# Optimization experiments

Measured on AMD Instinct MI355X. Metric: run time of the kernel, lower is better.

Reference implementation:

```python
import jax, jax.numpy as jnp
import numpy as np

K = 20                      # kNN size (init kwarg k)
_BN_S = 1.0 / np.sqrt(1.0 + 1e-5)  # BatchNorm eval with running var=1, mean=0


def _edge_conv(f, W1, b1, g, be, W2, b2):
    # f: [B,N,C]. DynamicEdgeConv: kNN in feature space (self included, as in
    # torch_cluster.knn), message = MLP([x_i, x_j - x_i]), max aggregation.
    sq = jnp.sum(f * f, -1)
    d = sq[:, :, None] + sq[:, None, :] - 2.0 * jnp.einsum('bnc,bmc->bnm', f, f)
    _, idx = jax.lax.top_k(-d, K)                      # [B,N,K]
    fj = jax.vmap(lambda fb, ib: fb[ib])(f, idx)       # [B,N,K,C] neighbor gather
    fi = jnp.broadcast_to(f[:, :, None, :], fj.shape)
    msg = jnp.concatenate([fi, fj - fi], -1)           # [B,N,K,2C]
    h = jax.nn.relu((msg @ W1 + b1) * (g * _BN_S) + be)  # Linear -> BN(eval) -> ReLU
    h = h @ W2 + b2                                    # plain last MLP layer
    return jnp.max(h, axis=2)                          # max over K neighbors


def _forward(x, pos,
             c1_W1, c1_b1, c1_g, c1_be, c1_W2, c1_b2,
             c2_W1, c2_b1, c2_g, c2_be, c2_W2, c2_b2,
             c3_W1, c3_b1, c3_g, c3_be, c3_W2, c3_b2,
             m_W1, m_b1, m_W2, m_b2, m_W3, m_b3, m_W4, m_b4):
    x0 = jnp.concatenate([x, pos], -1)                 # [B,N,6]
    x1 = _edge_conv(x0, c1_W1, c1_b1, c1_g, c1_be, c1_W2, c1_b2)
    x2 = _edge_conv(x1, c2_W1, c2_b1, c2_g, c2_be, c2_W2, c2_b2)
    x3 = _edge_conv(x2, c3_W1, c3_b1, c3_g, c3_be, c3_W2, c3_b2)
    h = jnp.concatenate([x1, x2, x3], -1)              # [B,N,192]
    # head MLP: norm=None, dropout inactive at inference, plain last layer
    h = jax.nn.relu(h @ m_W1 + m_b1)
    h = jax.nn.relu(h @ m_W2 + m_b2)
    h = jax.nn.relu(h @ m_W3 + m_b3)
    out = h @ m_W4 + m_b4                              # [B,N,40]
    return jax.nn.log_softmax(out, -1)


def setup_inputs() -> dict:
    key = jax.random.key(0)
    ks = iter(jax.random.split(key, 40))

    def lin(cin, cout):
        W = jax.random.normal(next(ks), (cin, cout), jnp.float32) / np.sqrt(cin)
        b = jnp.zeros((cout,), jnp.float32)
        return W, b

    inp = {}
    inp['x'] = jax.random.normal(next(ks), (8, 4096, 3), jnp.float32)
    inp['pos'] = jax.random.normal(next(ks), (8, 4096, 3), jnp.float32)
    for i, cin in zip((1, 2, 3), (12, 128, 128)):      # 2*in_channels of each conv
        W1, b1 = lin(cin, 64)
        W2, b2 = lin(64, 64)
        inp[f'c{i}_W1'], inp[f'c{i}_b1'] = W1, b1
        inp[f'c{i}_g'] = jnp.ones((64,), jnp.float32)
        inp[f'c{i}_be'] = jnp.zeros((64,), jnp.float32)
        inp[f'c{i}_W2'], inp[f'c{i}_b2'] = W2, b2
    dims = [192, 1024, 256, 128, 40]
    for j in range(4):
        W, b = lin(dims[j], dims[j + 1])
        inp[f'm_W{j + 1}'], inp[f'm_b{j + 1}'] = W, b
    return inp


def reference(x, pos,
              c1_W1, c1_b1, c1_g, c1_be, c1_W2, c1_b2,
              c2_W1, c2_b1, c2_g, c2_be, c2_W2, c2_b2,
              c3_W1, c3_b1, c3_g, c3_be, c3_W2, c3_b2,
              m_W1, m_b1, m_W2, m_b2, m_W3, m_b3, m_W4, m_b4):
    return _forward(x, pos,
                    c1_W1, c1_b1, c1_g, c1_be, c1_W2, c1_b2,
                    c2_W1, c2_b1, c2_g, c2_be, c2_W2, c2_b2,
                    c3_W1, c3_b1, c3_g, c3_be, c3_W2, c3_b2,
                    m_W1, m_b1, m_W2, m_b2, m_W3, m_b3, m_W4, m_b4)
```

## Files before the change

### kernel.cpp

```cpp
#include <hip/hip_runtime.h>
#include <math.h>

#define KNN 20
#define NPTS 4096
#define NB 8

__device__ __forceinline__ bool lexless(float d1, int i1, float d2, int i2) {
    return d1 < d2 || (d1 == d2 && i1 < i2);
}

__global__ __launch_bounds__(256) void concat_kernel(const float* __restrict__ x,
                                                     const float* __restrict__ pos,
                                                     float* __restrict__ f0, int total) {
    int p = blockIdx.x * 256 + threadIdx.x;
    if (p < total) {
        f0[(size_t)p*6 + 0] = x[(size_t)p*3 + 0];
        f0[(size_t)p*6 + 1] = x[(size_t)p*3 + 1];
        f0[(size_t)p*6 + 2] = x[(size_t)p*3 + 2];
        f0[(size_t)p*6 + 3] = pos[(size_t)p*3 + 0];
        f0[(size_t)p*6 + 4] = pos[(size_t)p*3 + 1];
        f0[(size_t)p*6 + 5] = pos[(size_t)p*3 + 2];
    }
}

template<int C>
__global__ __launch_bounds__(256) void norm_kernel(const float* __restrict__ f, int ldf,
                                                   float* __restrict__ norms, int total) {
    int p = blockIdx.x * 256 + threadIdx.x;
    if (p >= total) return;
    const float* fp = f + (size_t)p * ldf;
    float s = 0.f;
    if constexpr ((C & 3) == 0) {
#pragma unroll
        for (int k = 0; k < C; k += 4) {
            float4 v = *(const float4*)(fp + k);
            s = fmaf(v.x, v.x, s); s = fmaf(v.y, v.y, s);
            s = fmaf(v.z, v.z, s); s = fmaf(v.w, v.w, s);
        }
    } else {
#pragma unroll
        for (int k = 0; k < C; ++k) s = fmaf(fp[k], fp[k], s);
    }
    norms[p] = s;
}

#define KCHAIN(ck_) do {                                                 \
    unsigned long long kc = (ck_);                                       \
    _Pragma("unroll")                                                    \
    for (int t = 0; t < KNN; ++t) {                                      \
        bool sw = kc < bk[t];                                            \
        unsigned long long nn = sw ? kc : bk[t];                         \
        unsigned long long oo = sw ? bk[t] : kc;                         \
        bk[t] = nn; kc = oo;                                             \
    }                                                                    \
} while (0)

#define PACKK(dv_, jv_, out_) do {                                       \
    unsigned pu = __float_as_uint(dv_);                                  \
    pu = (pu == 0x80000000u) ? 0u : pu;                    \
    pu ^= (unsigned)((int)pu >> 31) | 0x80000000u;                       \
    (out_) = ((unsigned long long)pu << 32) | (unsigned)(jv_);           \
} while (0)

#define PUSHF(dv_, jg_) do {                                             \
    if ((dv_) <= thr) {                                                  \
        pd5 = pd4; pj5 = pj4; pd4 = pd3; pj4 = pj3;                      \
        pd3 = pd2; pj3 = pj2; pd2 = pd1; pj2 = pj1;                      \
        pd1 = pd0; pj1 = pj0; pd0 = (dv_); pj0 = (jg_); ++cnt;           \
    }                                                                    \
} while (0)

#define FLUSHF() do {                                                    \
    if (cnt > 0) { unsigned long long k0_; PACKK(pd0, pj0, k0_); KCHAIN(k0_); } \
    if (cnt > 1) { unsigned long long k1_; PACKK(pd1, pj1, k1_); KCHAIN(k1_); } \
    if (cnt > 2) { unsigned long long k2_; PACKK(pd2, pj2, k2_); KCHAIN(k2_); } \
    if (cnt > 3) { unsigned long long k3_; PACKK(pd3, pj3, k3_); KCHAIN(k3_); } \
    if (cnt > 4) { unsigned long long k4_; PACKK(pd4, pj4, k4_); KCHAIN(k4_); } \
    if (cnt > 5) { unsigned long long k5_; PACKK(pd5, pj5, k5_); KCHAIN(k5_); } \
    cnt = 0;                                                             \
    unsigned hu_ = (unsigned)(bk[KNN - 1] >> 32);                        \
    atomicMin(&thrQ[q], hu_);                                            \
    hu_ = (hu_ & 0x80000000u) ? (hu_ ^ 0x80000000u) : ~hu_;              \
    thr = __uint_as_float(hu_);                                          \
} while (0)

#define KMERGE(ptr_) do {                                                \
    const unsigned long long* mp = (ptr_);                               \
    _Pragma("unroll 1")                                                  \
    for (int tm = 0; tm < KNN; ++tm) {                                   \
        unsigned long long mk = mp[tm];                                  \
        if (mk >= bk[KNN - 1]) break;                                    \
        KCHAIN(mk);                                                      \
    }                                                                    \
} while (0)

#define KSENTINEL 0xFF800000FFFFFFFFULL

template<int C>
__global__ __launch_bounds__(128, 2) void knn_tile_kernel(const float* __restrict__ f, int ldf,
                                                          const float* __restrict__ norms,
                                                          int* __restrict__ idx) {
    const int qb    = blockIdx.x * 32;
    const int b     = qb >> 12;
    const int qloc0 = qb & (NPTS - 1);
    const int tid   = threadIdx.x;
    const int q     = tid & 31;
    const int sub   = tid >> 5;
    const int tx    = tid & 15;
    const int ty    = tid >> 4;

    union __align__(16) SM {
        struct {
            float Qs[C][32];
            float Cs[C][64];
            float Ds[32][68];
        } a;
        unsigned long long md[32][2 * KNN + 1];
    };
    __shared__ SM sm;
    __shared__ unsigned thrQ[32];

    const float* fb = f + (size_t)b * NPTS * ldf;
    const float* nb = norms + (size_t)b * NPTS;

    if (tid < 32) thrQ[tid] = 0xFFFFFFFFu;

    if constexpr ((C & 15) == 0) {
        int m = tid >> 2, ko = (tid & 3) * 4;
        const float* src = fb + (size_t)(qloc0 + m) * ldf;
#pragma unroll
        for (int k4 = ko; k4 < C; k4 += 16) {
            float4 v = *(const float4*)(src + k4);
            sm.a.Qs[k4 + 0][m] = v.x; sm.a.Qs[k4 + 1][m] = v.y;
            sm.a.Qs[k4 + 2][m] = v.z; sm.a.Qs[k4 + 3][m] = v.w;
        }
    } else {
        for (int e = tid; e < C * 32; e += 128) {
            int k = e >> 5, m = e & 31;
            sm.a.Qs[k][m] = fb[(size_t)(qloc0 + m) * ldf + k];
        }
    }

    const float4 qnv = *(const float4*)(nb + qloc0 + ty * 4);
    const float qnr[4] = {qnv.x, qnv.y, qnv.z, qnv.w};

    unsigned long long bk[KNN];
#pragma unroll
    for (int t = 0; t < KNN; ++t) bk[t] = KSENTINEL;
    float thr = INFINITY;
    float pd0 = 0.f, pd1 = 0.f, pd2 = 0.f, pd3 = 0.f, pd4 = 0.f, pd5 = 0.f;
    int   pj0 = 0, pj1 = 0, pj2 = 0, pj3 = 0, pj4 = 0, pj5 = 0;
    int   cnt = 0;

    auto stageC = [&](int j0) {
        if constexpr ((C & 7) == 0) {
            int jj = tid >> 1, ko = (tid & 1) * 4;
            const float* src = fb + (size_t)(j0 + jj) * ldf;
#pragma unroll
            for (int k4 = ko; k4 < C; k4 += 8) {
                float4 v = *(const float4*)(src + k4);
                sm.a.Cs[k4 + 0][jj] = v.x; sm.a.Cs[k4 + 1][jj] = v.y;
                sm.a.Cs[k4 + 2][jj] = v.z; sm.a.Cs[k4 + 3][jj] = v.w;
            }
        } else {
            for (int e = tid; e < C * 64; e += 128) {
                int k = e >> 6, j = e & 63;
                sm.a.Cs[k][j] = fb[(size_t)(j0 + j) * ldf + k];
            }
        }
    };

    auto gemmT = [&](int j0) {
        float acc[4][4] = {};
#pragma unroll 8
        for (int kk = 0; kk < C; ++kk) {
            float4 av = *(const float4*)&sm.a.Qs[kk][ty * 4];
            float4 bv = *(const float4*)&sm.a.Cs[kk][tx * 4];
            float a[4] = {av.x, av.y, av.z, av.w};
            float bb[4] = {bv.x, bv.y, bv.z, bv.w};
#pragma unroll
            for (int i = 0; i < 4; ++i)
#pragma unroll
                for (int j = 0; j < 4; ++j) acc[i][j] = fmaf(a[i], bb[j], acc[i][j]);
        }
        const float4 cnv = *(const float4*)(nb + j0 + tx * 4);
#pragma unroll
        for (int i = 0; i < 4; ++i) {
            float4 o;
            o.x = fmaf(-2.0f, acc[i][0], qnr[i] + cnv.x);
            o.y = fmaf(-2.0f, acc[i][1], qnr[i] + cnv.y);
            o.z = fmaf(-2.0f, acc[i][2], qnr[i] + cnv.z);
            o.w = fmaf(-2.0f, acc[i][3], qnr[i] + cnv.w);
            *(float4*)&sm.a.Ds[ty * 4 + i][tx * 4] = o;
        }
    };

    auto scanT = [&](int j0) {
        {
            unsigned su = thrQ[q];
            unsigned hu = (su & 0x80000000u) ? (su ^ 0x80000000u) : ~su;
            thr = fminf(thr, __uint_as_float(hu));
        }
        const int jb = sub * 16;
        const float4 v0 = *(const float4*)&sm.a.Ds[q][jb + 0];
        const float4 v1 = *(const float4*)&sm.a.Ds[q][jb + 4];
        const float4 v2 = *(const float4*)&sm.a.Ds[q][jb + 8];
        const float4 v3 = *(const float4*)&sm.a.Ds[q][jb + 12];
        const int jg = j0 + jb;
        PUSHF(v0.x, jg + 0);  PUSHF(v0.y, jg + 1);
        PUSHF(v0.z, jg + 2);  PUSHF(v0.w, jg + 3);  if (__any(cnt >= 3)) FLUSHF();
        PUSHF(v1.x, jg + 4);  PUSHF(v1.y, jg + 5);
        PUSHF(v1.z, jg + 6);  PUSHF(v1.w, jg + 7);  if (__any(cnt >= 3)) FLUSHF();
        PUSHF(v2.x, jg + 8);  PUSHF(v2.y, jg + 9);
        PUSHF(v2.z, jg + 10); PUSHF(v2.w, jg + 11); if (__any(cnt >= 3)) FLUSHF();
        PUSHF(v3.x, jg + 12); PUSHF(v3.y, jg + 13);
        PUSHF(v3.z, jg + 14); PUSHF(v3.w, jg + 15);
        if (__any(cnt > 0)) FLUSHF();
    };

    stageC(0);
    __syncthreads();
    gemmT(0);
    __syncthreads();
#pragma unroll 1
    for (int t = 1; t < NPTS / 64; ++t) {
        stageC(t * 64);
        scanT((t - 1) * 64);
        __syncthreads();
        gemmT(t * 64);
        __syncthreads();
    }
    scanT(NPTS - 64);
    if (__any(cnt > 0)) FLUSHF();

    __syncthreads();
    if (sub >= 2) {
#pragma unroll
        for (int t = 0; t < KNN; ++t) sm.md[q][(sub - 2) * KNN + t] = bk[t];
    }
    __syncthreads();
    if (sub < 2) KMERGE(&sm.md[q][sub * KNN]);
    __syncthreads();
    if (sub == 1) {
#pragma unroll
        for (int t = 0; t < KNN; ++t) sm.md[q][t] = bk[t];
    }
    __syncthreads();
    if (sub == 0) {
        KMERGE(&sm.md[q][0]);
        int* op = idx + (size_t)(qb + q) * KNN;
#pragma unroll
        for (int t = 0; t < KNN; ++t) op[t] = (int)bk[t];
    }
}

template<int C>
__global__ __launch_bounds__(64) void edgeconv_kernel(
    const float* __restrict__ f, int ldf,
    const int* __restrict__ idx,
    const float* __restrict__ W1, const float* __restrict__ b1,
    const float* __restrict__ g,  const float* __restrict__ be,
    const float* __restrict__ W2, const float* __restrict__ b2,
    float* __restrict__ out, int ldo) {
    const int p = blockIdx.x;
    const int b = p >> 12;
    const int i = p & (NPTS - 1);
    const int c = threadIdx.x;
    __shared__ __align__(16) float fi_s[C];
    __shared__ __align__(16) float fj_s[KNN][C];
    __shared__ __align__(16) float h1_s[KNN][64];
    __shared__ int nidx[KNN];
    const float* fb = f + (size_t)b * NPTS * ldf;
    if (c < KNN) nidx[c] = idx[(size_t)p * KNN + c];
    if (c < C)   fi_s[c] = fb[(size_t)i * ldf + c];
    __syncthreads();
#pragma unroll
    for (int j = 0; j < KNN; ++j)
        if (c < C) fj_s[j][c] = fb[(size_t)nidx[j] * ldf + c];
    __syncthreads();
    float fir[C];
#pragma unroll
    for (int k = 0; k < C; ++k) fir[k] = fi_s[k];

    const float bn_s = (float)(1.0 / sqrt(1.0 + 1e-5));
    const float bnscale = g[c] * bn_s;
    float base = b1[c];
#pragma unroll
    for (int k = 0; k < C; ++k) base = fmaf(fir[k], W1[k * 64 + c], base);
    float acc[KNN];
#pragma unroll
    for (int j = 0; j < KNN; ++j) acc[j] = base;

    if constexpr ((C & 3) == 0) {
#pragma unroll
        for (int k = 0; k < C; k += 4) {
            float w0 = W1[(C + k + 0) * 64 + c];
            float w1 = W1[(C + k + 1) * 64 + c];
            float w2 = W1[(C + k + 2) * 64 + c];
            float w3 = W1[(C + k + 3) * 64 + c];
            float f0 = fir[k + 0], f1 = fir[k + 1], f2 = fir[k + 2], f3 = fir[k + 3];
#pragma unroll
            for (int j = 0; j < KNN; ++j) {
                float4 v = *(const float4*)&fj_s[j][k];
                acc[j] = fmaf(v.x - f0, w0, acc[j]);
                acc[j] = fmaf(v.y - f1, w1, acc[j]);
                acc[j] = fmaf(v.z - f2, w2, acc[j]);
                acc[j] = fmaf(v.w - f3, w3, acc[j]);
            }
        }
    } else {
#pragma unroll
        for (int k = 0; k < C; ++k) {
            float w = W1[(C + k) * 64 + c];
            float fik = fir[k];
#pragma unroll
            for (int j = 0; j < KNN; ++j) acc[j] = fmaf(fj_s[j][k] - fik, w, acc[j]);
        }
    }
    float bec = be[c];
#pragma unroll
    for (int j = 0; j < KNN; ++j) h1_s[j][c] = fmaxf(fmaf(acc[j], bnscale, bec), 0.f);
    __syncthreads();

    float acc2[KNN];
    float b2c = b2[c];
#pragma unroll
    for (int j = 0; j < KNN; ++j) acc2[j] = b2c;
#pragma unroll
    for (int k = 0; k < 64; k += 4) {
        float w0 = W2[(k + 0) * 64 + c];
        float w1 = W2[(k + 1) * 64 + c];
        float w2 = W2[(k + 2) * 64 + c];
        float w3 = W2[(k + 3) * 64 + c];
#pragma unroll
        for (int j = 0; j < KNN; ++j) {
            float4 v = *(const float4*)&h1_s[j][k];
            acc2[j] = fmaf(v.x, w0, acc2[j]);
            acc2[j] = fmaf(v.y, w1, acc2[j]);
            acc2[j] = fmaf(v.z, w2, acc2[j]);
            acc2[j] = fmaf(v.w, w3, acc2[j]);
        }
    }
    float m = acc2[0];
#pragma unroll
    for (int j = 1; j < KNN; ++j) m = fmaxf(m, acc2[j]);
    out[(size_t)p * ldo + c] = m;
}

template<bool RELU>
__global__ __launch_bounds__(256, 2) void gemm_kernel(
    const float* __restrict__ A, int lda,
    const float* __restrict__ W,
    const float* __restrict__ bias,
    float* __restrict__ Cc, int ldc,
    int N, int K) {
    const int BM = 128, BN = 128, BK = 16;
    __shared__ __align__(16) float As[16][128 + 4];
    __shared__ __align__(16) float Bs[16][128 + 4];
    const int bm = blockIdx.y * BM;
    const int bn = blockIdx.x * BN;
    const int tid = threadIdx.x;
    const int tx = tid & 15, ty = tid >> 4;
    float acc[8][8] = {};
    for (int k0 = 0; k0 < K; k0 += BK) {
        {
            int r = tid >> 2;
            int kq = (tid & 3) * 4;
#pragma unroll
            for (int h = 0; h < 2; ++h) {
                int rr = r + h * 64;
                float4 v = *(const float4*)(A + (size_t)(bm + rr) * lda + k0 + kq);
                As[kq + 0][rr] = v.x; As[kq + 1][rr] = v.y;
                As[kq + 2][rr] = v.z; As[kq + 3][rr] = v.w;
            }
        }
        {
            int kk = tid >> 4;
            int n8 = (tid & 15) * 8;
            float4 v0 = *(const float4*)(W + (size_t)(k0 + kk) * N + bn + n8);
            float4 v1 = *(const float4*)(W + (size_t)(k0 + kk) * N + bn + n8 + 4);
            *(float4*)&Bs[kk][n8] = v0;
            *(float4*)&Bs[kk][n8 + 4] = v1;
        }
        __syncthreads();
#pragma unroll
        for (int kk = 0; kk < BK; ++kk) {
            float4 a0 = *(const float4*)&As[kk][ty * 8];
            float4 a1 = *(const float4*)&As[kk][ty * 8 + 4];
            float4 b0 = *(const float4*)&Bs[kk][tx * 8];
            float4 b1 = *(const float4*)&Bs[kk][tx * 8 + 4];
            float a[8] = {a0.x, a0.y, a0.z, a0.w, a1.x, a1.y, a1.z, a1.w};
            float bb[8] = {b0.x, b0.y, b0.z, b0.w, b1.x, b1.y, b1.z, b1.w};
#pragma unroll
            for (int i = 0; i < 8; ++i)
#pragma unroll
                for (int j = 0; j < 8; ++j) acc[i][j] = fmaf(a[i], bb[j], acc[i][j]);
        }
        __syncthreads();
    }
    const float4 bi0 = *(const float4*)(bias + bn + tx * 8);
    const float4 bi1 = *(const float4*)(bias + bn + tx * 8 + 4);
    const float bb[8] = {bi0.x, bi0.y, bi0.z, bi0.w, bi1.x, bi1.y, bi1.z, bi1.w};
#pragma unroll
    for (int i = 0; i < 8; ++i) {
        int m = bm + ty * 8 + i;
        float4 o0, o1;
        o0.x = acc[i][0] + bb[0]; o0.y = acc[i][1] + bb[1];
        o0.z = acc[i][2] + bb[2]; o0.w = acc[i][3] + bb[3];
        o1.x = acc[i][4] + bb[4]; o1.y = acc[i][5] + bb[5];
        o1.z = acc[i][6] + bb[6]; o1.w = acc[i][7] + bb[7];
        if (RELU) {
            o0.x = fmaxf(o0.x, 0.f); o0.y = fmaxf(o0.y, 0.f);
            o0.z = fmaxf(o0.z, 0.f); o0.w = fmaxf(o0.w, 0.f);
            o1.x = fmaxf(o1.x, 0.f); o1.y = fmaxf(o1.y, 0.f);
            o1.z = fmaxf(o1.z, 0.f); o1.w = fmaxf(o1.w, 0.f);
        }
        *(float4*)(Cc + (size_t)m * ldc + bn + tx * 8) = o0;
        *(float4*)(Cc + (size_t)m * ldc + bn + tx * 8 + 4) = o1;
    }
}

__global__ __launch_bounds__(64) void head_kernel(const float* __restrict__ h3,
                                                  const float* __restrict__ W4,
                                                  const float* __restrict__ b4,
                                                  float* __restrict__ out) {
    const int p = blockIdx.x;
    const int lane = threadIdx.x;
    const float* hp = h3 + (size_t)p * 128;
    float v = -INFINITY;
    if (lane < 40) {
        float acc = b4[lane];
#pragma unroll
        for (int k = 0; k < 128; ++k) acc = fmaf(hp[k], W4[k * 40 + lane], acc);
        v = acc;
    }
    float mx = v;
#pragma unroll
    for (int s = 1; s < 64; s <<= 1) mx = fmaxf(mx, __shfl_xor(mx, s));
    float e = (lane < 40) ? expf(v - mx) : 0.0f;
    float se = e;
#pragma unroll
    for (int s = 1; s < 64; s <<= 1) se += __shfl_xor(se, s);
    if (lane < 40) out[(size_t)p * 40 + lane] = v - mx - logf(se);
}

extern "C" void kernel_launch(void* const* d_in, const int* in_sizes, int n_in,
                              void* d_out, int out_size, void* d_ws, size_t ws_size,
                              hipStream_t stream) {
    (void)in_sizes; (void)n_in; (void)out_size;
    const float* x     = (const float*)d_in[0];
    const float* pos   = (const float*)d_in[1];
    const float* c1_W1 = (const float*)d_in[2];
    const float* c1_b1 = (const float*)d_in[3];
    const float* c1_g  = (const float*)d_in[4];
    const float* c1_be = (const float*)d_in[5];
    const float* c1_W2 = (const float*)d_in[6];
    const float* c1_b2 = (const float*)d_in[7];
    const float* c2_W1 = (const float*)d_in[8];
    const float* c2_b1 = (const float*)d_in[9];
    const float* c2_g  = (const float*)d_in[10];
    const float* c2_be = (const float*)d_in[11];
    const float* c2_W2 = (const float*)d_in[12];
    const float* c2_b2 = (const float*)d_in[13];
    const float* c3_W1 = (const float*)d_in[14];
    const float* c3_b1 = (const float*)d_in[15];
    const float* c3_g  = (const float*)d_in[16];
    const float* c3_be = (const float*)d_in[17];
    const float* c3_W2 = (const float*)d_in[18];
    const float* c3_b2 = (const float*)d_in[19];
    const float* m_W1  = (const float*)d_in[20];
    const float* m_b1  = (const float*)d_in[21];
    const float* m_W2  = (const float*)d_in[22];
    const float* m_b2  = (const float*)d_in[23];
    const float* m_W3  = (const float*)d_in[24];
    const float* m_b3  = (const float*)d_in[25];
    const float* m_W4  = (const float*)d_in[26];
    const float* m_b4  = (const float*)d_in[27];
    float* out = (float*)d_out;

    const int TOT = NB * NPTS;

    float* ws   = (float*)d_ws;
    float* f0   = ws;
    int*   idxb = (int*)(ws + 196608);
    float* feat = ws + 196608 + 655360;

    const size_t basef  = 196608 + 655360 + 6291456;
    const size_t availf = ws_size / 4;
    int MC = 4096;
    if (availf >= basef + (size_t)32768 * 1408) MC = 32768;
    else if (availf >= basef + (size_t)16384 * 1408) MC = 16384;
    else if (availf >= basef + (size_t)8192 * 1408) MC = 8192;

    float* h1   = feat + 6291456;
    float* h2   = h1 + (size_t)MC * 1024;
    float* h3   = h2 + (size_t)MC * 256;
    float* nrm  = h1;

    concat_kernel<<<(TOT + 255) / 256, 256, 0, stream>>>(x, pos, f0, TOT);

    norm_kernel<6><<<(TOT + 255) / 256, 256, 0, stream>>>(f0, 6, nrm, TOT);
    knn_tile_kernel<6><<<TOT / 32, 128, 0, stream>>>(f0, 6, nrm, idxb);
    edgeconv_kernel<6><<<TOT, 64, 0, stream>>>(f0, 6, idxb,
        c1_W1, c1_b1, c1_g, c1_be, c1_W2, c1_b2, feat + 0, 192);

    norm_kernel<64><<<(TOT + 255) / 256, 256, 0, stream>>>(feat + 0, 192, nrm, TOT);
    knn_tile_kernel<64><<<TOT / 32, 128, 0, stream>>>(feat + 0, 192, nrm, idxb);
    edgeconv_kernel<64><<<TOT, 64, 0, stream>>>(feat + 0, 192, idxb,
        c2_W1, c2_b1, c2_g, c2_be, c2_W2, c2_b2, feat + 64, 192);

    norm_kernel<64><<<(TOT + 255) / 256, 256, 0, stream>>>(feat + 64, 192, nrm, TOT);
    knn_tile_kernel<64><<<TOT / 32, 128, 0, stream>>>(feat + 64, 192, nrm, idxb);
    edgeconv_kernel<64><<<TOT, 64, 0, stream>>>(feat + 64, 192, idxb,
        c3_W1, c3_b1, c3_g, c3_be, c3_W2, c3_b2, feat + 128, 192);

    for (int mc = 0; mc < TOT; mc += MC) {
        gemm_kernel<true><<<dim3(1024 / 128, MC / 128), 256, 0, stream>>>(
            feat + (size_t)mc * 192, 192, m_W1, m_b1, h1, 1024, 1024, 192);
        gemm_kernel<true><<<dim3(256 / 128, MC / 128), 256, 0, stream>>>(
            h1, 1024, m_W2, m_b2, h2, 256, 256, 1024);
        gemm_kernel<true><<<dim3(128 / 128, MC / 128), 256, 0, stream>>>(
            h2, 256, m_W3, m_b3, h3, 128, 128, 256);
        head_kernel<<<MC, 64, 0, stream>>>(h3, m_W4, m_b4, out + (size_t)mc * 40);
    }
}
```

Baseline: 2.416 ms.

## Factor edge-conv first layer into per-point GEMM plus neighbor gather

Splits the first linear layer of edge convs 2 and 3 algebraically: [x_i, x_j - x_i]W1 = x_i(Wa - Wb) + x_j Wb. A repack kernel builds a combined weight, one GEMM computes both per-point terms for all points, and a new edge kernel gathers the neighbor term instead of recomputing a 128x64 product per edge. This removes most first-layer FLOPs but adds a GH buffer carved from workspace, which could overlap the head buffers, and two extra launches.

```diff
diff --git a/kernel.cpp b/kernel.cpp
--- a/kernel.cpp
+++ b/kernel.cpp
@@ -320,6 +320,71 @@
     float bec = be[c];
 #pragma unroll
     for (int j = 0; j < KNN; ++j) h1_s[j][c] = fmaxf(fmaf(acc[j], bnscale, bec), 0.f);
+    __syncthreads();
+
+    float acc2[KNN];
+    float b2c = b2[c];
+#pragma unroll
+    for (int j = 0; j < KNN; ++j) acc2[j] = b2c;
+#pragma unroll
+    for (int k = 0; k < 64; k += 4) {
+        float w0 = W2[(k + 0) * 64 + c];
+        float w1 = W2[(k + 1) * 64 + c];
+        float w2 = W2[(k + 2) * 64 + c];
+        float w3 = W2[(k + 3) * 64 + c];
+#pragma unroll
+        for (int j = 0; j < KNN; ++j) {
+            float4 v = *(const float4*)&h1_s[j][k];
+            acc2[j] = fmaf(v.x, w0, acc2[j]);
+            acc2[j] = fmaf(v.y, w1, acc2[j]);
+            acc2[j] = fmaf(v.z, w2, acc2[j]);
+            acc2[j] = fmaf(v.w, w3, acc2[j]);
+        }
+    }
+    float m = acc2[0];
+#pragma unroll
+    for (int j = 1; j < KNN; ++j) m = fmaxf(m, acc2[j]);
+    out[(size_t)p * ldo + c] = m;
+}
+
+__global__ __launch_bounds__(256) void repack_w1_kernel(const float* __restrict__ W1,
+                                                        const float* __restrict__ b1,
+                                                        float* __restrict__ Wp,
+                                                        float* __restrict__ bp) {
+    int t = blockIdx.x * 256 + threadIdx.x;
+    if (t < 64 * 64) {
+        int k = t >> 6, c = t & 63;
+        Wp[k * 128 + c]      = W1[k * 64 + c];
+        Wp[k * 128 + 64 + c] = W1[(64 + k) * 64 + c];
+    }
+    if (t < 128) bp[t] = (t < 64) ? b1[t] : 0.f;
+}
+
+__global__ __launch_bounds__(64) void edgeconv_fact_kernel(
+    const float* __restrict__ GH,
+    const int* __restrict__ idx,
+    const float* __restrict__ g,  const float* __restrict__ be,
+    const float* __restrict__ W2, const float* __restrict__ b2,
+    float* __restrict__ out, int ldo) {
+    const int p = blockIdx.x;
+    const int b = p >> 12;
+    const int c = threadIdx.x;
+    __shared__ __align__(16) float h1_s[KNN][64];
+    __shared__ int nidx[KNN];
+    if (c < KNN) nidx[c] = idx[(size_t)p * KNN + c];
+    const float H = GH[(size_t)p * 128 + c];
+    const float G = GH[(size_t)p * 128 + 64 + c];
+    const float hb = H - G;
+    const float bn_s = (float)(1.0 / sqrt(1.0 + 1e-5));
+    const float bnscale = g[c] * bn_s;
+    const float bec = be[c];
+    const float* GHb = GH + (size_t)b * NPTS * 128 + 64;
+    __syncthreads();
+#pragma unroll
+    for (int j = 0; j < KNN; ++j) {
+        float gj = GHb[(size_t)nidx[j] * 128 + c];
+        h1_s[j][c] = fmaxf(fmaf(hb + gj, bnscale, bec), 0.f);
+    }
     __syncthreads();
 
     float acc2[KNN];
@@ -496,6 +561,9 @@
     float* h2   = h1 + (size_t)MC * 1024;
     float* h3   = h2 + (size_t)MC * 256;
     float* nrm  = h1;
+    float* GH   = h1 + 131072;
+    float* Wp   = GH + (size_t)TOT * 128;
+    float* bp   = Wp + 8192;
 
     concat_kernel<<<(TOT + 255) / 256, 256, 0, stream>>>(x, pos, f0, TOT);
 
@@ -506,13 +574,19 @@
 
     norm_kernel<64><<<(TOT + 255) / 256, 256, 0, stream>>>(feat + 0, 192, nrm, TOT);
     knn_tile_kernel<64><<<TOT / 32, 128, 0, stream>>>(feat + 0, 192, nrm, idxb);
-    edgeconv_kernel<64><<<TOT, 64, 0, stream>>>(feat + 0, 192, idxb,
-        c2_W1, c2_b1, c2_g, c2_be, c2_W2, c2_b2, feat + 64, 192);
+    repack_w1_kernel<<<16, 256, 0, stream>>>(c2_W1, c2_b1, Wp, bp);
+    gemm_kernel<false><<<dim3(1, TOT / 128), 256, 0, stream>>>(
+        feat + 0, 192, Wp, bp, GH, 128, 128, 64);
+    edgeconv_fact_kernel<<<TOT, 64, 0, stream>>>(GH, idxb,
+        c2_g, c2_be, c2_W2, c2_b2, feat + 64, 192);
 
     norm_kernel<64><<<(TOT + 255) / 256, 256, 0, stream>>>(feat + 64, 192, nrm, TOT);
     knn_tile_kernel<64><<<TOT / 32, 128, 0, stream>>>(feat + 64, 192, nrm, idxb);
-    edgeconv_kernel<64><<<TOT, 64, 0, stream>>>(feat + 64, 192, idxb,
-        c3_W1, c3_b1, c3_g, c3_be, c3_W2, c3_b2, feat + 128, 192);
+    repack_w1_kernel<<<16, 256, 0, stream>>>(c3_W1, c3_b1, Wp, bp);
+    gemm_kernel<false><<<dim3(1, TOT / 128), 256, 0, stream>>>(
+        feat + 64, 192, Wp, bp, GH, 128, 128, 64);
+    edgeconv_fact_kernel<<<TOT, 64, 0, stream>>>(GH, idxb,
+        c3_g, c3_be, c3_W2, c3_b2, feat + 128, 192);
 
     for (int mc = 0; mc < TOT; mc += MC) {
         gemm_kernel<true><<<dim3(1024 / 128, MC / 128), 256, 0, stream>>>(
```

After: 2.212 ms. 8.4% less time.
